# Kernel tuning notes

Measured on AMD Instinct MI355X. Metric: run time of the kernel, lower is better.

Reference implementation:

```python
import jax, jax.numpy as jnp
import numpy as np

B, DIM, H, W = 8, 512, 32, 32
HC, WC = 32, 32
NH, DH = 8, 64
DE = NH * DH  # dim_embed = 512


def setup_inputs() -> dict:
    key = jax.random.key(0)
    ks = jax.random.split(key, 6)
    return {
        "x": jax.random.normal(ks[0], (B, DIM, H, W), jnp.float32),
        "context": jax.random.normal(ks[1], (B, DIM, HC, WC), jnp.float32),
        "gamma": jnp.ones((DIM, 1, 1), jnp.float32),
        "w_q": jax.random.normal(ks[2], (DE, DIM), jnp.float32) * 0.02,
        "w_k": jax.random.normal(ks[3], (DE, DIM), jnp.float32) * 0.02,
        "w_v": jax.random.normal(ks[4], (DE, DIM), jnp.float32) * 0.02,
        "w_proj": jax.random.normal(ks[5], (DIM, DE), jnp.float32) * 0.02,
    }


def _rms_norm(t, gamma, scale):
    # torch F.normalize(dim=1): x / max(||x||_2, 1e-12) along channel axis
    nrm = jnp.sqrt(jnp.sum(t * t, axis=1, keepdims=True))
    return t / jnp.maximum(nrm, 1e-12) * scale * gamma


def _split_heads(t, h, w):
    # 'b (c n) h w -> (b n) (h w) c' with c=DH, n=NH
    b = t.shape[0]
    t = t.reshape(b, DH, NH, h, w).transpose(0, 2, 3, 4, 1)  # b n h w c
    return t.reshape(b * NH, h * w, DH)


def reference(x, context, gamma, w_q, w_k, w_v, w_proj):
    scale = float(DIM) ** 0.5
    xn = _rms_norm(x, gamma, scale)
    # faithful to source bug: self.norm (not norm_context) applied to context
    cn = _rms_norm(context, gamma, scale)

    q = jnp.einsum('bchw,oc->bohw', xn, w_q)
    k = jnp.einsum('bchw,oc->bohw', cn, w_k)
    v = jnp.einsum('bchw,oc->bohw', cn, w_v)

    q = _split_heads(q, H, W)      # (B*NH, H*W, DH)
    k = _split_heads(k, HC, WC)    # (B*NH, HC*WC, DH)
    v = _split_heads(v, HC, WC)

    qk = jnp.einsum('bmc,bnc->bmn', q, k) * (float(DH) ** -0.5)
    attn = jnp.einsum('bmn,bnc->bmc', jax.nn.softmax(qk, axis=-1) + 1e-8, v) + 1e-8

    # '(b n) (h w) c -> b (c n) h w'
    attn = attn.reshape(B, NH, H, W, DH).transpose(0, 4, 1, 2, 3).reshape(B, DE, H, W)
    return jnp.einsum('bchw,oc->bohw', attn, w_proj)
```

## Files before the change

kernel.cpp:

```cpp
#include <hip/hip_runtime.h>
#include <hip/hip_bf16.h>


typedef _Float16 half8v __attribute__((ext_vector_type(8)));
typedef __fp16 fp16x2 __attribute__((ext_vector_type(2)));
typedef __attribute__((ext_vector_type(4))) float float4v;
typedef __attribute__((ext_vector_type(16))) float float16v;
typedef __attribute__((ext_vector_type(2))) int int2v;

__device__ inline ushort f2h(float f) {
  union { _Float16 h; ushort u; } cv;
  cv.h = (_Float16)f;
  return cv.u;
}

__device__ inline unsigned pk2(float a, float b) {
  union { fp16x2 h; unsigned u; } cv;
  cv.h = __builtin_amdgcn_cvt_pkrtz(a, b);
  return cv.u;
}

__device__ inline void stage16(const void* g, void* l) {
  __builtin_amdgcn_global_load_lds(
      (const __attribute__((address_space(1))) unsigned*)g,
      (__attribute__((address_space(3))) unsigned*)l, 16, 0, 0);
}

__device__ inline void permswap(unsigned& a, unsigned& b) {
#if __has_builtin(__builtin_amdgcn_permlane32_swap)
  int2v r = __builtin_amdgcn_permlane32_swap((int)a, (int)b, false, false);
  a = (unsigned)r[0];
  b = (unsigned)r[1];
#else
  unsigned pa = (unsigned)__shfl_xor((int)a, 32, 64);
  unsigned pb = (unsigned)__shfl_xor((int)b, 32, 64);
  bool hb = (threadIdx.x & 32) != 0;
  unsigned na = hb ? pb : a;
  unsigned nb = hb ? b : pa;
  a = na;
  b = nb;
#endif
}

__global__ __launch_bounds__(256) void prep_kernel(
    const float* __restrict__ x, const float* __restrict__ ctx,
    const float* __restrict__ wq, const float* __restrict__ wk,
    const float* __restrict__ wv, const float* __restrict__ wp,
    const float* __restrict__ gamma, ushort* __restrict__ xT,
    ushort* __restrict__ cT, float* __restrict__ sx, float* __restrict__ sc,
    ushort* __restrict__ wf) {
  __shared__ ushort tile[32 * 512];
  __shared__ float part[32][32];
  const int bid = blockIdx.x;
  const int t = threadIdx.x;

  if (bid < 512) {
    const int tensor = bid >> 8;
    const int b = (bid >> 5) & 7;
    const int pos0 = (bid & 31) << 5;
    const float* src = tensor ? ctx : x;
    ushort* dstT = tensor ? cT : xT;
    float* dstS = tensor ? sc : sx;
    unsigned* tile32 = (unsigned*)tile;

    const int pcq = t & 7;
    const int crg = t >> 3;
    float ssq[4] = {0.f, 0.f, 0.f, 0.f};

    const float* srcb = src + ((size_t)b * 512) * 1024 + pos0;
    for (int p = 0; p < 8; ++p) {
      const int cr0 = p * 64 + crg * 2;
      float4 v0 = *(const float4*)&srcb[(size_t)cr0 * 1024 + pcq * 4];
      float4 v1 = *(const float4*)&srcb[(size_t)(cr0 + 1) * 1024 + pcq * 4];
      ssq[0] += v0.x * v0.x + v1.x * v1.x;
      ssq[1] += v0.y * v0.y + v1.y * v1.y;
      ssq[2] += v0.z * v0.z + v1.z * v1.z;
      ssq[3] += v0.w * v0.w + v1.w * v1.w;
      const int cp = cr0 >> 1;
      float e0[4] = {v0.x, v0.y, v0.z, v0.w};
      float e1[4] = {v1.x, v1.y, v1.z, v1.w};
#pragma unroll
      for (int j = 0; j < 4; ++j) {
        const int posl = pcq * 4 + j;
        unsigned pk = (unsigned)f2h(e0[j]) | ((unsigned)f2h(e1[j]) << 16);
        tile32[posl * 256 + (cp ^ posl)] = pk;
      }
    }
#pragma unroll
    for (int j = 0; j < 4; ++j) part[crg][pcq * 4 + j] = ssq[j];
    __syncthreads();
    if (t < 32) {
      float s = 0.f;
#pragma unroll
      for (int g2 = 0; g2 < 32; ++g2) s += part[g2][t];
      dstS[b * 1024 + pos0 + t] =
          22.627416997969522f / fmaxf(sqrtf(s), 1e-12f);
    }
    ushort* ob = dstT + ((size_t)b * 1024 + pos0) * 512;
#pragma unroll
    for (int ii = 0; ii < 8; ++ii) {
      const int m = t + ii * 256;
      const int posl = m >> 6, c16 = m & 63;
      uint4 u;
      u.x = tile32[posl * 256 + ((c16 * 4 + 0) ^ posl)];
      u.y = tile32[posl * 256 + ((c16 * 4 + 1) ^ posl)];
      u.z = tile32[posl * 256 + ((c16 * 4 + 2) ^ posl)];
      u.w = tile32[posl * 256 + ((c16 * 4 + 3) ^ posl)];
      *(uint4*)&ob[(size_t)posl * 512 + c16 * 8] = u;
    }
  } else {
    const int wbid = bid - 512;
    const int m = wbid >> 7;
    const float* W = (m == 0) ? wq : (m == 1) ? wk : (m == 2) ? wv : wp;
    const int r = (wbid & 127) * 4 + (t >> 6);
    const int c8 = (t & 63) * 8;
    ushort h[8];
    if (m < 3) {
      const int o = ((r & 63) << 3) + (r >> 6);
      const float* wr_ = &W[(size_t)o * 512 + c8];
#pragma unroll
      for (int j = 0; j < 8; ++j) h[j] = f2h(wr_[j] * gamma[c8 + j]);
    } else {
#pragma unroll
      for (int j = 0; j < 8; ++j) {
        const int cc = c8 + j;
        const int cs = ((cc & 63) << 3) + (cc >> 6);
        h[j] = f2h(W[(size_t)r * 512 + cs]);
      }
    }
    ushort* dst = &wf[((size_t)m * 512 + r) * 512 + c8];
    uint4 u;
    u.x = (unsigned)h[0] | ((unsigned)h[1] << 16);
    u.y = (unsigned)h[2] | ((unsigned)h[3] << 16);
    u.z = (unsigned)h[4] | ((unsigned)h[5] << 16);
    u.w = (unsigned)h[6] | ((unsigned)h[7] << 16);
    *(uint4*)dst = u;
  }
}

__global__ __launch_bounds__(256, 2) void qkv_kernel(
    const ushort* __restrict__ xT, const ushort* __restrict__ cT,
    const ushort* __restrict__ wf, const float* __restrict__ sx,
    const float* __restrict__ sc, ushort* __restrict__ qh,
    ushort* __restrict__ kh, ushort* __restrict__ vt) {
  const int z = blockIdx.z;
  const int proj = z % 3;
  const int b = z / 3;
  const ushort* XT = (proj == 0) ? xT : cT;
  const float* S = (proj == 0) ? sx : sc;
  const ushort* WF = wf + (size_t)proj * 262144;
  const int pos0 = blockIdx.x << 7;
  const int o0 = blockIdx.y << 7;

  __shared__ __align__(16) unsigned char lds[65536];
  unsigned char* Al = lds;
  unsigned char* Bl = lds + 32768;

  const int t = threadIdx.x, w = t >> 6, lane = t & 63;
  const int g = lane >> 4, l15 = lane & 15;
  const int wr = w >> 1, wc = w & 1;
  const int srow_ = lane >> 3;
  const int sslot16 = ((lane & 7) ^ srow_) << 4;

  const unsigned char* Asrc =
      (const unsigned char*)(XT + ((size_t)b * 1024 + pos0) * 512);
  const unsigned char* Bsrc = (const unsigned char*)(WF + (size_t)o0 * 512);

#define QSTAGE(buf, kk)                                                     \
  do {                                                                      \
    _Pragma("unroll") for (int i = 0; i < 4; ++i) {                         \
      const int j = (w << 2) + i;                                           \
      stage16(Asrc + (size_t)((j << 3) + srow_) * 1024 + (kk)*128 + sslot16,\
              Al + (buf)*16384 + (j << 10));                                \
      stage16(Bsrc + (size_t)((j << 3) + srow_) * 1024 + (kk)*128 + sslot16,\
              Bl + (buf)*16384 + (j << 10));                                \
    }                                                                       \
  } while (0)

  float4v acc[4][4];
#pragma unroll
  for (int i = 0; i < 4; ++i)
#pragma unroll
    for (int j2 = 0; j2 < 4; ++j2) acc[i][j2] = (float4v){0.f, 0.f, 0.f, 0.f};

  QSTAGE(0, 0);
  __syncthreads();

  for (int kk = 0; kk < 8; ++kk) {
    const int cur = kk & 1;
    if (kk < 7) QSTAGE(cur ^ 1, kk + 1);
    const unsigned char* At = Al + cur * 16384;
    const unsigned char* Bt = Bl + cur * 16384;
    half8v af[4][2], bf[4][2];
#pragma unroll
    for (int mt = 0; mt < 4; ++mt) {
      const int row = (wr << 6) + (mt << 4) + l15;
      const unsigned char* rb = At + row * 128;
      af[mt][0] = *(const half8v*)(rb + (((g) ^ (row & 7)) << 4));
      af[mt][1] = *(const half8v*)(rb + (((4 + g) ^ (row & 7)) << 4));
    }
#pragma unroll
    for (int nt = 0; nt < 4; ++nt) {
      const int row = (wc << 6) + (nt << 4) + l15;
      const unsigned char* rb = Bt + row * 128;
      bf[nt][0] = *(const half8v*)(rb + (((g) ^ (row & 7)) << 4));
      bf[nt][1] = *(const half8v*)(rb + (((4 + g) ^ (row & 7)) << 4));
    }
    if (proj < 2) {
#pragma unroll
      for (int mt = 0; mt < 4; ++mt)
#pragma unroll
        for (int nt = 0; nt < 4; ++nt) {
          acc[mt][nt] = __builtin_amdgcn_mfma_f32_16x16x32_f16(
              af[mt][0], bf[nt][0], acc[mt][nt], 0, 0, 0);
          acc[mt][nt] = __builtin_amdgcn_mfma_f32_16x16x32_f16(
              af[mt][1], bf[nt][1], acc[mt][nt], 0, 0, 0);
        }
    } else {
#pragma unroll
      for (int mt = 0; mt < 4; ++mt)
#pragma unroll
        for (int nt = 0; nt < 4; ++nt) {
          acc[mt][nt] = __builtin_amdgcn_mfma_f32_16x16x32_f16(
              bf[nt][0], af[mt][0], acc[mt][nt], 0, 0, 0);
          acc[mt][nt] = __builtin_amdgcn_mfma_f32_16x16x32_f16(
              bf[nt][1], af[mt][1], acc[mt][nt], 0, 0, 0);
        }
    }
    __syncthreads();
  }
#undef QSTAGE

  if (proj < 2) {
    ushort* Out = (proj == 0) ? qh : kh;
    const float qsc = (proj == 0) ? 0.125f : 1.0f;
#pragma unroll
    for (int mt = 0; mt < 4; ++mt) {
      const int posb = pos0 + (wr << 6) + (mt << 4) + (g << 2);
      float4 sv4 = *(const float4*)&S[b * 1024 + posb];
      float sarr[4] = {sv4.x * qsc, sv4.y * qsc, sv4.z * qsc, sv4.w * qsc};
#pragma unroll
      for (int nt = 0; nt < 4; ++nt) {
        const int oo = o0 + (wc << 6) + (nt << 4) + l15;
#pragma unroll
        for (int r = 0; r < 4; ++r) {
          float val = acc[mt][nt][r] * sarr[r];
          Out[((size_t)(b * 1024 + posb + r)) * 512 + oo] = f2h(val);
        }
      }
    }
  } else {
#pragma unroll
    for (int mt = 0; mt < 4; ++mt) {
      const int pos = pos0 + (wr << 6) + (mt << 4) + l15;
      const float sval = S[b * 1024 + pos];
#pragma unroll
      for (int nt = 0; nt < 4; ++nt) {
        const int ob = o0 + (wc << 6) + (nt << 4) + (g << 2);
#pragma unroll
        for (int r = 0; r < 4; ++r) {
          const int oo = ob + r;
          vt[((size_t)(b * 512 + oo)) * 1024 + pos] = f2h(acc[mt][nt][r] * sval);
        }
      }
    }
  }
}

__global__ __launch_bounds__(512, 2) void attn_kernel(
    const ushort* __restrict__ qh, const ushort* __restrict__ kh,
    const ushort* __restrict__ vt, ushort* __restrict__ am) {
  __shared__ __align__(16) unsigned char lds[32768];

  const int bid = blockIdx.x;
  const int bh = ((bid & 7) << 3) + (bid >> 5);
  const int b = bh >> 3, n = bh & 7;
  const int mbase = ((bid >> 3) & 3) << 8;
  const int t = threadIdx.x;
  const int w = t >> 6;
  const int lane = t & 63;
  const int l31 = lane & 31;
  const int hi = lane >> 5;
  const int swz = (l31 & 7) << 4;

  half8v qf[4];
  const size_t qrow = (size_t)b * 1024 + mbase + w * 32 + l31;
#pragma unroll
  for (int kc = 0; kc < 4; ++kc)
    qf[kc] = *(const half8v*)(qh + qrow * 512 + n * 64 + kc * 16 + hi * 8);

  float16v o[2];
#pragma unroll
  for (int d2 = 0; d2 < 2; ++d2)
#pragma unroll
    for (int e = 0; e < 16; ++e) o[d2][e] = 0.f;
  float rsum = 0.f;

  const unsigned char* kgb =
      (const unsigned char*)kh + (size_t)b * 1048576 + n * 128;
  const unsigned char* vgb =
      (const unsigned char*)vt + (size_t)b * 1048576 + n * 131072;
  const int kro = (t >> 3) * 1024 + (((t & 7) ^ ((t >> 3) & 7)) << 4);
  const int vro = (t >> 3) * 2048 + (((t & 7) ^ ((t >> 3) & 7)) << 4);

#define ASTAGE(buf, kt)                                                   \
  do {                                                                    \
    stage16(kgb + (size_t)(kt)*65536 + kro, lds + (buf)*8192 + t * 16);   \
    stage16(vgb + (size_t)(kt)*128 + vro,                                 \
            lds + 16384 + (buf)*8192 + t * 16);                           \
  } while (0)

  ASTAGE(0, 0);
  __syncthreads();

  for (int kt = 0; kt < 16; ++kt) {
    const int cur = kt & 1;
    if (kt < 15) ASTAGE(cur ^ 1, kt + 1);
    const unsigned char* Kc = lds + cur * 8192;
    const unsigned char* Vc = lds + 16384 + cur * 8192;

    half8v vf[4][2];
#pragma unroll
    for (int ks = 0; ks < 4; ++ks)
#pragma unroll
      for (int d2 = 0; d2 < 2; ++d2)
        vf[ks][d2] = *(const half8v*)(Vc + (l31 + 32 * d2) * 128 +
                                      ((hi * 16 + ks * 32) ^ swz));

#pragma unroll
    for (int kt2 = 0; kt2 < 2; ++kt2) {
      half8v kf[4];
#pragma unroll
      for (int kc = 0; kc < 4; ++kc)
        kf[kc] = *(const half8v*)(Kc + (l31 + 32 * kt2) * 128 +
                                  ((hi * 16 + kc * 32) ^ swz));
      float16v st;
#pragma unroll
      for (int e = 0; e < 16; ++e) st[e] = 0.f;
#pragma unroll
      for (int kc = 0; kc < 4; ++kc)
        st = __builtin_amdgcn_mfma_f32_32x32x16_f16(kf[kc], qf[kc], st, 0, 0,
                                                    0);
      float p[16];
#pragma unroll
      for (int r = 0; r < 16; ++r) p[r] = __expf(st[r]);
      rsum += (((p[0] + p[1]) + (p[2] + p[3])) +
               ((p[4] + p[5]) + (p[6] + p[7]))) +
              (((p[8] + p[9]) + (p[10] + p[11])) +
               ((p[12] + p[13]) + (p[14] + p[15])));
      unsigned wds[8];
#pragma unroll
      for (int j = 0; j < 8; ++j) wds[j] = pk2(p[2 * j], p[2 * j + 1]);
      permswap(wds[0], wds[2]);
      permswap(wds[1], wds[3]);
      permswap(wds[4], wds[6]);
      permswap(wds[5], wds[7]);
      union { half8v h; unsigned u[4]; } pf0, pf1;
      pf0.u[0] = wds[0]; pf0.u[1] = wds[1];
      pf0.u[2] = wds[2]; pf0.u[3] = wds[3];
      pf1.u[0] = wds[4]; pf1.u[1] = wds[5];
      pf1.u[2] = wds[6]; pf1.u[3] = wds[7];
#pragma unroll
      for (int d2 = 0; d2 < 2; ++d2) {
        o[d2] = __builtin_amdgcn_mfma_f32_32x32x16_f16(
            pf0.h, vf[kt2 * 2 + 0][d2], o[d2], 0, 0, 0);
        o[d2] = __builtin_amdgcn_mfma_f32_32x32x16_f16(
            pf1.h, vf[kt2 * 2 + 1][d2], o[d2], 0, 0, 0);
      }
    }
    __syncthreads();
  }
#undef ASTAGE

  const float inv = 1.0f / (rsum + __shfl_xor(rsum, 32, 64));

#pragma unroll
  for (int r = 0; r < 16; ++r) {
    const int qloc = (r & 3) + 8 * (r >> 2) + 4 * hi;
    const float iv = __shfl(inv, qloc, 64);
    const size_t rowbase =
        ((size_t)(b * 1024 + mbase + w * 32 + qloc)) * 512 + n * 64 + l31;
#pragma unroll
    for (int d2 = 0; d2 < 2; ++d2) {
      am[rowbase + 32 * d2] = f2h(o[d2][r] * iv);
    }
  }
}

__global__ __launch_bounds__(256, 3) void proj_kernel(
    const ushort* __restrict__ am, const ushort* __restrict__ wf3,
    float* __restrict__ out) {
  const int b = blockIdx.z;
  const int pos0 = blockIdx.x << 7;
  const int o0 = blockIdx.y << 6;

  __shared__ __align__(16) unsigned char lds[49152];
  unsigned char* Al = lds;
  unsigned char* Bl = lds + 16384;

  const int t = threadIdx.x, w = t >> 6, lane = t & 63;
  const int g = lane >> 4, l15 = lane & 15;
  const int wr = w >> 1, wc = w & 1;

  const unsigned char* Asrc = (const unsigned char*)(wf3 + (size_t)o0 * 512);
  const unsigned char* Bsrc =
      (const unsigned char*)(am + ((size_t)b * 1024 + pos0) * 512);

#define PSTAGE(buf, kk)                                                      \
  do {                                                                       \
    _Pragma("unroll") for (int i = 0; i < 2; ++i) {                          \
      const int u = t + (i << 8);                                            \
      const int row = u >> 3;                                                \
      stage16(Asrc + (size_t)row * 1024 + (kk)*128 +                         \
                  (((u & 7) ^ (row & 7)) << 4),                              \
              Al + (buf)*8192 + u * 16);                                     \
    }                                                                        \
    _Pragma("unroll") for (int i = 0; i < 4; ++i) {                          \
      const int u = t + (i << 8);                                            \
      const int row = u >> 3;                                                \
      stage16(Bsrc + (size_t)row * 1024 + (kk)*128 +                         \
                  (((u & 7) ^ (row & 7)) << 4),                              \
              Bl + (buf)*16384 + u * 16);                                    \
    }                                                                        \
  } while (0)

  float4v acc[2][4];
#pragma unroll
  for (int i = 0; i < 2; ++i)
#pragma unroll
    for (int j2 = 0; j2 < 4; ++j2) acc[i][j2] = (float4v){0.f, 0.f, 0.f, 0.f};

  PSTAGE(0, 0);
  __syncthreads();

  for (int kk = 0; kk < 8; ++kk) {
    const int cur = kk & 1;
    if (kk < 7) PSTAGE(cur ^ 1, kk + 1);
    const unsigned char* At = Al + cur * 8192;
    const unsigned char* Bt = Bl + cur * 16384;
    half8v af[2][2], bf[4][2];
#pragma unroll
    for (int mt = 0; mt < 2; ++mt) {
      const int row = (wr << 5) + (mt << 4) + l15;
      const unsigned char* rb = At + row * 128;
      af[mt][0] = *(const half8v*)(rb + (((g) ^ (row & 7)) << 4));
      af[mt][1] = *(const half8v*)(rb + (((4 + g) ^ (row & 7)) << 4));
    }
#pragma unroll
    for (int nt = 0; nt < 4; ++nt) {
      const int row = (wc << 6) + (nt << 4) + l15;
      const unsigned char* rb = Bt + row * 128;
      bf[nt][0] = *(const half8v*)(rb + (((g) ^ (row & 7)) << 4));
      bf[nt][1] = *(const half8v*)(rb + (((4 + g) ^ (row & 7)) << 4));
    }
#pragma unroll
    for (int mt = 0; mt < 2; ++mt)
#pragma unroll
      for (int nt = 0; nt < 4; ++nt) {
        acc[mt][nt] = __builtin_amdgcn_mfma_f32_16x16x32_f16(
            af[mt][0], bf[nt][0], acc[mt][nt], 0, 0, 0);
        acc[mt][nt] = __builtin_amdgcn_mfma_f32_16x16x32_f16(
            af[mt][1], bf[nt][1], acc[mt][nt], 0, 0, 0);
      }
    __syncthreads();
  }
#undef PSTAGE

#pragma unroll
  for (int mt = 0; mt < 2; ++mt) {
    const int ob = o0 + (wr << 5) + (mt << 4) + (g << 2);
#pragma unroll
    for (int nt = 0; nt < 4; ++nt) {
      const int pos = pos0 + (wc << 6) + (nt << 4) + l15;
#pragma unroll
      for (int r = 0; r < 4; ++r) {
        out[((size_t)(b * 512 + ob + r)) * 1024 + pos] = acc[mt][nt][r];
      }
    }
  }
}

extern "C" void kernel_launch(void* const* d_in, const int* in_sizes, int n_in,
                              void* d_out, int out_size, void* d_ws,
                              size_t ws_size, hipStream_t stream) {
  const float* x = (const float*)d_in[0];
  const float* ctx = (const float*)d_in[1];
  const float* gamma = (const float*)d_in[2];
  const float* wq = (const float*)d_in[3];
  const float* wk = (const float*)d_in[4];
  const float* wv = (const float*)d_in[5];
  const float* wp = (const float*)d_in[6];
  float* out = (float*)d_out;

  char* ws = (char*)d_ws;
  float* sx = (float*)(ws);
  float* sc = (float*)(ws + 32768);
  ushort* xT = (ushort*)(ws + 65536);
  ushort* cT = (ushort*)(ws + 65536 + 8388608);
  ushort* wf = (ushort*)(ws + 65536 + 16777216);
  ushort* qh = (ushort*)(ws + 65536 + 18874368);
  ushort* kh = (ushort*)(ws + 65536 + 27262976);
  ushort* vt = (ushort*)(ws + 65536 + 35651584);
  ushort* am = xT;

  prep_kernel<<<1024, 256, 0, stream>>>(x, ctx, wq, wk, wv, wp, gamma, xT, cT,
                                        sx, sc, wf);
  qkv_kernel<<<dim3(8, 4, 24), 256, 0, stream>>>(xT, cT, wf, sx, sc, qh, kh,
                                                 vt);
  attn_kernel<<<256, 512, 0, stream>>>(qh, kh, vt, am);
  proj_kernel<<<dim3(8, 8, 8), 256, 0, stream>>>(am, wf + 3 * 262144, out);
}
```

Baseline: 62.83 us.

## Stage full K tile in LDS once and load V directly from global

The attention kernel now copies the whole 1024x64 K block for its head into a 128 KB LDS buffer up front and drops the double-buffered per-iteration staging and barriers. V fragments are read straight from global memory each iteration instead of going through LDS. This removes the 16 per-iteration __syncthreads and the V LDS round-trip. In exchange, occupancy drops to one 512-thread block per CU, V loads are exposed global latency inside the loop, and there is no overlap between K staging and compute.

```diff
diff --git a/kernel.cpp b/kernel.cpp
--- a/kernel.cpp
+++ b/kernel.cpp
@@ -267,10 +267,10 @@
   }
 }
 
-__global__ __launch_bounds__(512, 2) void attn_kernel(
+__global__ __launch_bounds__(512, 1) void attn_kernel(
     const ushort* __restrict__ qh, const ushort* __restrict__ kh,
     const ushort* __restrict__ vt, ushort* __restrict__ am) {
-  __shared__ __align__(16) unsigned char lds[32768];
+  __shared__ __align__(16) unsigned char lds[131072];
 
   const int bid = blockIdx.x;
   const int bh = ((bid & 7) << 3) + (bid >> 5);
@@ -298,34 +298,27 @@
 
   const unsigned char* kgb =
       (const unsigned char*)kh + (size_t)b * 1048576 + n * 128;
-  const unsigned char* vgb =
-      (const unsigned char*)vt + (size_t)b * 1048576 + n * 131072;
-  const int kro = (t >> 3) * 1024 + (((t & 7) ^ ((t >> 3) & 7)) << 4);
-  const int vro = (t >> 3) * 2048 + (((t & 7) ^ ((t >> 3) & 7)) << 4);
-
-#define ASTAGE(buf, kt)                                                   \
-  do {                                                                    \
-    stage16(kgb + (size_t)(kt)*65536 + kro, lds + (buf)*8192 + t * 16);   \
-    stage16(vgb + (size_t)(kt)*128 + vro,                                 \
-            lds + 16384 + (buf)*8192 + t * 16);                           \
-  } while (0)
-
-  ASTAGE(0, 0);
+#pragma unroll
+  for (int i = 0; i < 16; ++i) {
+    const int u = t + (i << 9);
+    const int row = u >> 3;
+    stage16(kgb + (size_t)row * 1024 + (((u & 7) ^ (row & 7)) << 4),
+            lds + u * 16);
+  }
   __syncthreads();
 
+  const ushort* vbase = vt + ((size_t)(b * 512 + n * 64)) * 1024;
+
   for (int kt = 0; kt < 16; ++kt) {
-    const int cur = kt & 1;
-    if (kt < 15) ASTAGE(cur ^ 1, kt + 1);
-    const unsigned char* Kc = lds + cur * 8192;
-    const unsigned char* Vc = lds + 16384 + cur * 8192;
+    const unsigned char* Kc = lds + kt * 8192;
 
     half8v vf[4][2];
 #pragma unroll
     for (int ks = 0; ks < 4; ++ks)
 #pragma unroll
       for (int d2 = 0; d2 < 2; ++d2)
-        vf[ks][d2] = *(const half8v*)(Vc + (l31 + 32 * d2) * 128 +
-                                      ((hi * 16 + ks * 32) ^ swz));
+        vf[ks][d2] = *(const half8v*)(vbase + (size_t)(l31 + 32 * d2) * 1024 +
+                                      kt * 64 + ks * 16 + hi * 8);
 
 #pragma unroll
     for (int kt2 = 0; kt2 < 2; ++kt2) {
@@ -368,9 +361,7 @@
             pf1.h, vf[kt2 * 2 + 1][d2], o[d2], 0, 0, 0);
       }
     }
-    __syncthreads();
-  }
-#undef ASTAGE
+  }
 
   const float inv = 1.0f / (rsum + __shfl_xor(rsum, 32, 64));
 
```

Measured after the change: 75.56 us. +20.3%, slower.
